# Optimization experiments

Measured on AMD Instinct MI355X. Metric: run time of the kernel, lower is better.

## Reference

```python
import jax, jax.numpy as jnp
import numpy as np

D = 6
EPS = 1e-5


def layer_norm(x, w, b):
    m = jnp.mean(x, axis=-1, keepdims=True)
    v = jnp.mean(jnp.square(x - m), axis=-1, keepdims=True)
    return (x - m) * jax.lax.rsqrt(v + EPS) * w + b


def setup_inputs() -> dict:
    key = jax.random.key(0)
    ks = jax.random.split(key, 8)
    B, S = 8192, 128
    scale = 0.2
    return {
        "x": jax.random.normal(ks[0], (B, S, D), jnp.float32),
        "ln1_w": jnp.ones((D,), jnp.float32),
        "ln1_b": jnp.zeros((D,), jnp.float32),
        "wqkv": jax.random.normal(ks[1], (D, 3 * D), jnp.float32) * scale,
        "bqkv": jnp.zeros((3 * D,), jnp.float32),
        "wo": jax.random.normal(ks[2], (D, D), jnp.float32) * scale,
        "bo": jnp.zeros((D,), jnp.float32),
        "ln2_w": jnp.ones((D,), jnp.float32),
        "ln2_b": jnp.zeros((D,), jnp.float32),
        "w1": jax.random.normal(ks[3], (D, D), jnp.float32) * scale,
        "b1": jnp.zeros((D,), jnp.float32),
        "w2": jax.random.normal(ks[4], (D, D), jnp.float32) * scale,
        "b2": jnp.zeros((D,), jnp.float32),
    }


def reference(x, ln1_w, ln1_b, wqkv, bqkv, wo, bo, ln2_w, ln2_b, w1, b1, w2, b2):
    B, S, _ = x.shape
    # --- attention sub-block: x = x + attn(ln1(x)) ---
    h = layer_norm(x, ln1_w, ln1_b)                      # [B,S,D]
    qkv = h @ wqkv + bqkv                                # [B,S,3D]
    q, k, v = jnp.split(qkv, 3, axis=-1)
    scores = jnp.einsum('bqd,bkd->bqk', q, k) / jnp.sqrt(jnp.asarray(D, x.dtype))
    causal = jnp.tril(jnp.ones((S, S), bool))            # [S,S]
    scores = jnp.where(causal, scores, jnp.asarray(-1e9, x.dtype))
    attn = jax.nn.softmax(scores, axis=-1)               # [B,S,S]
    o = jnp.einsum('bqk,bkd->bqd', attn, v) @ wo + bo
    x = x + o
    # --- FFN sub-block: x = x + W2 @ gelu(W1 @ ln2(x)) ---
    h2 = layer_norm(x, ln2_w, ln2_b)
    ff = jax.nn.gelu(h2 @ w1 + b1, approximate=False) @ w2 + b2
    return x + ff
```

## Files before the change

### kernel.cpp

```cpp
#include <hip/hip_runtime.h>
#include <cmath>


typedef float    v2f  __attribute__((ext_vector_type(2)));
typedef float    f4v  __attribute__((ext_vector_type(4)));
typedef short    s4v  __attribute__((ext_vector_type(4)));
typedef uint32_t u2   __attribute__((ext_vector_type(2)));

constexpr int D = 6;
constexpr int S = 128;
#define EPS 1e-5f
#define RSQRT_D 0.4082482904638631f
#define LOG2E   1.4426950408889634f

#define EXP2F(x) __builtin_amdgcn_exp2f(x)
#define RCPF(x)  __builtin_amdgcn_rcpf(x)
#define PKFMA(a, b, c) __builtin_elementwise_fma((a), (b), (c))

union UA { uint32_t u[2]; u2 h; s4v v; };

__device__ __forceinline__ uint32_t pkbf(float hi, float lo) {
    return __builtin_amdgcn_perm(__builtin_bit_cast(uint32_t, hi),
                                 __builtin_bit_cast(uint32_t, lo),
                                 0x07060302u);
}
__device__ __forceinline__ uint16_t bf16t(float x) {
    return (uint16_t)(__builtin_bit_cast(uint32_t, x) >> 16);
}

__device__ __forceinline__ f4v mfma16(s4v a, s4v b, f4v c) {
#if __has_builtin(__builtin_amdgcn_mfma_f32_16x16x16bf16_1k)
    return __builtin_amdgcn_mfma_f32_16x16x16bf16_1k(a, b, c, 0, 0, 0);
#else
    f4v d;
    asm volatile("v_mfma_f32_16x16x16_bf16 %0, %1, %2, %3\n\t"
                 "s_nop 7\n\ts_nop 2"
                 : "=v"(d) : "v"(a), "v"(b), "v"(c));
    return d;
#endif
}

template<int QA, int QB>
__device__ __forceinline__ void attn_pair(
    const UA (&kf)[8], const UA (&vf)[8],
    const uint32_t (*qlds)[6], float (*obuf)[10],
    int l15, int lq, int aoff)
{
    UA qfA, qfB;
    qfA.h = *(const u2*)((const char*)&qlds[QA * 16 + l15][0] + aoff);
    qfB.h = *(const u2*)((const char*)&qlds[QB * 16 + l15][0] + aoff);
    const f4v z = {0.f, 0.f, 0.f, 0.f};
    f4v OA = z, OB = z;
    #pragma unroll
    for (int jt = 0; jt <= QB; ++jt) {
        f4v cB = mfma16(kf[jt].v, qfB.v, z);
        f4v cA;
        if (jt <= QA) cA = mfma16(kf[jt].v, qfA.v, z);
        float pB0 = EXP2F(cB[0]);
        float pB1 = EXP2F(cB[1]);
        float pB2 = EXP2F(cB[2]);
        float pB3 = EXP2F(cB[3]);
        if (jt == QB) {
            pB0 = (lq * 4 + 0 > l15) ? 0.f : pB0;
            pB1 = (lq * 4 + 1 > l15) ? 0.f : pB1;
            pB2 = (lq * 4 + 2 > l15) ? 0.f : pB2;
            pB3 = (lq * 4 + 3 > l15) ? 0.f : pB3;
        }
        UA paB;
        paB.u[0] = pkbf(pB1, pB0);
        paB.u[1] = pkbf(pB3, pB2);
        OB = mfma16(paB.v, vf[jt].v, OB);
        if (jt <= QA) {
            float pA0 = EXP2F(cA[0]);
            float pA1 = EXP2F(cA[1]);
            float pA2 = EXP2F(cA[2]);
            float pA3 = EXP2F(cA[3]);
            if (jt == QA) {
                pA0 = (lq * 4 + 0 > l15) ? 0.f : pA0;
                pA1 = (lq * 4 + 1 > l15) ? 0.f : pA1;
                pA2 = (lq * 4 + 2 > l15) ? 0.f : pA2;
                pA3 = (lq * 4 + 3 > l15) ? 0.f : pA3;
            }
            UA paA;
            paA.u[0] = pkbf(pA1, pA0);
            paA.u[1] = pkbf(pA3, pA2);
            OA = mfma16(paA.v, vf[jt].v, OA);
        }
    }
    if (l15 < 7) {
        #pragma unroll
        for (int r = 0; r < 4; ++r) {
            obuf[QA * 16 + lq * 4 + r][l15] = OA[r];
            obuf[QB * 16 + lq * 4 + r][l15] = OB[r];
        }
    }
}

__global__ __launch_bounds__(S, 6) void txblock_kernel(
    const float* __restrict__ x,
    const float* __restrict__ ln1_w, const float* __restrict__ ln1_b,
    const float* __restrict__ wqkv,  const float* __restrict__ bqkv,
    const float* __restrict__ wo,    const float* __restrict__ bo,
    const float* __restrict__ ln2_w, const float* __restrict__ ln2_b,
    const float* __restrict__ w1,    const float* __restrict__ b1,
    const float* __restrict__ w2,    const float* __restrict__ b2,
    float* __restrict__ out)
{
    __shared__ uint32_t qlds[S][6];
    __shared__ uint32_t klds[S][6];
    __shared__ uint16_t vt[8][S + 8];
    __shared__ float    obuf[S][10];

    const int b = blockIdx.x;
    const int s = threadIdx.x;
    const float* xrow = x + ((size_t)b * S + s) * D;
    float*      orow = out + ((size_t)b * S + s) * D;

    v2f xv01 = ((const v2f*)xrow)[0];
    v2f xv23 = ((const v2f*)xrow)[1];
    v2f xv45 = ((const v2f*)xrow)[2];
    float xv[D] = {xv01[0], xv01[1], xv23[0], xv23[1], xv45[0], xv45[1]};

    float m = 0.f;
    #pragma unroll
    for (int d = 0; d < D; ++d) m += xv[d];
    m *= (1.0f / D);
    float var = 0.f;
    #pragma unroll
    for (int d = 0; d < D; ++d) { float t = xv[d] - m; var += t * t; }
    var *= (1.0f / D);
    float rstd = rsqrtf(var + EPS);
    float h1[D];
    #pragma unroll
    for (int d = 0; d < D; ++d)
        h1[d] = (xv[d] - m) * rstd * ln1_w[d] + ln1_b[d];

    v2f aq[3], ak[3], av[3];
    #pragma unroll
    for (int jp = 0; jp < 3; ++jp) {
        aq[jp] = ((const v2f*)bqkv)[jp];
        ak[jp] = ((const v2f*)(bqkv + D))[jp];
        av[jp] = ((const v2f*)(bqkv + 2 * D))[jp];
    }
    #pragma unroll
    for (int d = 0; d < D; ++d) {
        const float* wrow = wqkv + d * 3 * D;
        v2f hd = {h1[d], h1[d]};
        #pragma unroll
        for (int jp = 0; jp < 3; ++jp) {
            aq[jp] = PKFMA(hd, ((const v2f*)wrow)[jp], aq[jp]);
            ak[jp] = PKFMA(hd, ((const v2f*)(wrow + D))[jp], ak[jp]);
            av[jp] = PKFMA(hd, ((const v2f*)(wrow + 2 * D))[jp], av[jp]);
        }
    }
    const v2f qscale = {RSQRT_D * LOG2E, RSQRT_D * LOG2E};

    #pragma unroll
    for (int jp = 0; jp < 3; ++jp) {
        v2f qs = aq[jp] * qscale;
        qlds[s][jp] = pkbf(qs[1], qs[0]);
        klds[s][jp] = pkbf(ak[jp][1], ak[jp][0]);
    }
    qlds[s][3] = 0; qlds[s][4] = 0; qlds[s][5] = 0;
    klds[s][3] = 0; klds[s][4] = 0; klds[s][5] = 0;
    vt[0][s] = bf16t(av[0][0]);
    vt[1][s] = bf16t(av[0][1]);
    vt[2][s] = bf16t(av[1][0]);
    vt[3][s] = bf16t(av[1][1]);
    vt[4][s] = bf16t(av[2][0]);
    vt[5][s] = bf16t(av[2][1]);
    vt[6][s] = 0x3F80;
    vt[7][s] = 0;
    __syncthreads();

    const int wv  = s >> 6;
    const int l15 = s & 15;
    const int lq  = (s >> 4) & 3;
    const int aoff = (lq < 2) ? lq * 8 : 16;
    const int vne  = (l15 < 7) ? l15 : 7;

    UA kf[8], vf[8];
    #pragma unroll
    for (int jt = 0; jt < 8; ++jt) {
        kf[jt].h = *(const u2*)((const char*)&klds[jt * 16 + l15][0] + aoff);
        vf[jt].h = *(const u2*)&vt[vne][jt * 16 + lq * 4];
    }

    if (wv == 0) {
        attn_pair<0, 7>(kf, vf, qlds, obuf, l15, lq, aoff);
        attn_pair<3, 4>(kf, vf, qlds, obuf, l15, lq, aoff);
    } else {
        attn_pair<1, 6>(kf, vf, qlds, obuf, l15, lq, aoff);
        attn_pair<2, 5>(kf, vf, qlds, obuf, l15, lq, aoff);
    }
    __syncthreads();

    v2f rx01 = ((const v2f*)xrow)[0];
    v2f rx23 = ((const v2f*)xrow)[1];
    v2f rx45 = ((const v2f*)xrow)[2];

    v2f o01 = *(const v2f*)&obuf[s][0];
    v2f o23 = *(const v2f*)&obuf[s][2];
    v2f o45 = *(const v2f*)&obuf[s][4];
    float invl = RCPF(obuf[s][6]);
    v2f il = {invl, invl};
    o01 *= il; o23 *= il; o45 *= il;
    float av6[D] = {o01[0], o01[1], o23[0], o23[1], o45[0], o45[1]};

    v2f xvp[3] = {rx01, rx23, rx45};
    v2f x2p[3];
    #pragma unroll
    for (int dp = 0; dp < 3; ++dp) {
        v2f o = ((const v2f*)bo)[dp];
        #pragma unroll
        for (int e = 0; e < D; ++e) {
            v2f we = ((const v2f*)(wo + e * D))[dp];
            v2f ae = {av6[e], av6[e]};
            o = PKFMA(ae, we, o);
        }
        x2p[dp] = o + xvp[dp];
    }
    float x2[D] = {x2p[0][0], x2p[0][1], x2p[1][0], x2p[1][1], x2p[2][0], x2p[2][1]};

    float m2 = 0.f;
    #pragma unroll
    for (int d = 0; d < D; ++d) m2 += x2[d];
    m2 *= (1.0f / D);
    float var2 = 0.f;
    #pragma unroll
    for (int d = 0; d < D; ++d) { float t = x2[d] - m2; var2 += t * t; }
    var2 *= (1.0f / D);
    float rstd2 = rsqrtf(var2 + EPS);
    float h2[D];
    #pragma unroll
    for (int d = 0; d < D; ++d)
        h2[d] = (x2[d] - m2) * rstd2 * ln2_w[d] + ln2_b[d];

    v2f ap[3];
    #pragma unroll
    for (int jp = 0; jp < 3; ++jp) {
        v2f a = ((const v2f*)b1)[jp];
        #pragma unroll
        for (int d = 0; d < D; ++d) {
            v2f wd = ((const v2f*)(w1 + d * D))[jp];
            v2f hd = {h2[d], h2[d]};
            a = PKFMA(hd, wd, a);
        }
        ap[jp] = a;
    }
    float g[D];
    #pragma unroll
    for (int j = 0; j < D; ++j) {
        float a = ap[j >> 1][j & 1];
        float t  = a * a;
        float in = fmaf(0.044715f * t, a, a);
        float e  = EXP2F(in * -2.3022229f);
        float r  = RCPF(1.0f + e);
        g[j] = a * r;
    }
    #pragma unroll
    for (int dp = 0; dp < 3; ++dp) {
        v2f a = ((const v2f*)b2)[dp];
        #pragma unroll
        for (int e = 0; e < D; ++e) {
            v2f we = ((const v2f*)(w2 + e * D))[dp];
            v2f ge = {g[e], g[e]};
            a = PKFMA(ge, we, a);
        }
        ((v2f*)orow)[dp] = x2p[dp] + a;
    }
}

extern "C" void kernel_launch(void* const* d_in, const int* in_sizes, int n_in,
                              void* d_out, int out_size, void* d_ws, size_t ws_size,
                              hipStream_t stream) {
    const float* x     = (const float*)d_in[0];
    const float* ln1_w = (const float*)d_in[1];
    const float* ln1_b = (const float*)d_in[2];
    const float* wqkv  = (const float*)d_in[3];
    const float* bqkv  = (const float*)d_in[4];
    const float* wo    = (const float*)d_in[5];
    const float* bo    = (const float*)d_in[6];
    const float* ln2_w = (const float*)d_in[7];
    const float* ln2_b = (const float*)d_in[8];
    const float* w1    = (const float*)d_in[9];
    const float* b1    = (const float*)d_in[10];
    const float* w2    = (const float*)d_in[11];
    const float* b2    = (const float*)d_in[12];
    float* out = (float*)d_out;

    const int B = in_sizes[0] / (S * D);
    txblock_kernel<<<B, S, 0, stream>>>(x, ln1_w, ln1_b, wqkv, bqkv, wo, bo,
                                        ln2_w, ln2_b, w1, b1, w2, b2, out);
}
```

Baseline: 115.4 us.

## Alias output buffer onto Q/K shared memory and raise occupancy target

The obuf shared array now reuses the Q/K LDS storage, with an extra barrier once Q and K fragments are in registers, so each block uses less LDS. V fragments are loaded from LDS inside the attention loop rather than held in registers, cutting register pressure. The launch-bounds minimum is raised from 6 to 8 blocks per CU. The goal is higher occupancy, at the cost of one more __syncthreads and repeated LDS reads of V.

```diff
diff --git a/kernel.cpp b/kernel.cpp
--- a/kernel.cpp
+++ b/kernel.cpp
@@ -42,17 +42,14 @@
 
 template<int QA, int QB>
 __device__ __forceinline__ void attn_pair(
-    const UA (&kf)[8], const UA (&vf)[8],
-    const uint32_t (*qlds)[6], float (*obuf)[10],
-    int l15, int lq, int aoff)
+    const UA (&kf)[8], const uint16_t (*vt)[S + 8], int vne,
+    UA qfA, UA qfB, float (*obuf)[10], int l15, int lq)
 {
-    UA qfA, qfB;
-    qfA.h = *(const u2*)((const char*)&qlds[QA * 16 + l15][0] + aoff);
-    qfB.h = *(const u2*)((const char*)&qlds[QB * 16 + l15][0] + aoff);
     const f4v z = {0.f, 0.f, 0.f, 0.f};
     f4v OA = z, OB = z;
     #pragma unroll
     for (int jt = 0; jt <= QB; ++jt) {
+        UA vf; vf.h = *(const u2*)&vt[vne][jt * 16 + lq * 4];
         f4v cB = mfma16(kf[jt].v, qfB.v, z);
         f4v cA;
         if (jt <= QA) cA = mfma16(kf[jt].v, qfA.v, z);
@@ -69,7 +66,7 @@
         UA paB;
         paB.u[0] = pkbf(pB1, pB0);
         paB.u[1] = pkbf(pB3, pB2);
-        OB = mfma16(paB.v, vf[jt].v, OB);
+        OB = mfma16(paB.v, vf.v, OB);
         if (jt <= QA) {
             float pA0 = EXP2F(cA[0]);
             float pA1 = EXP2F(cA[1]);
@@ -84,7 +81,7 @@
             UA paA;
             paA.u[0] = pkbf(pA1, pA0);
             paA.u[1] = pkbf(pA3, pA2);
-            OA = mfma16(paA.v, vf[jt].v, OA);
+            OA = mfma16(paA.v, vf.v, OA);
         }
     }
     if (l15 < 7) {
@@ -96,7 +93,7 @@
     }
 }
 
-__global__ __launch_bounds__(S, 6) void txblock_kernel(
+__global__ __launch_bounds__(S, 8) void txblock_kernel(
     const float* __restrict__ x,
     const float* __restrict__ ln1_w, const float* __restrict__ ln1_b,
     const float* __restrict__ wqkv,  const float* __restrict__ bqkv,
@@ -106,10 +103,9 @@
     const float* __restrict__ w2,    const float* __restrict__ b2,
     float* __restrict__ out)
 {
-    __shared__ uint32_t qlds[S][6];
-    __shared__ uint32_t klds[S][6];
+    __shared__ uint32_t qk[2][S][6];
     __shared__ uint16_t vt[8][S + 8];
-    __shared__ float    obuf[S][10];
+    float (*obuf)[10] = reinterpret_cast<float(*)[10]>(&qk[0][0][0]);
 
     const int b = blockIdx.x;
     const int s = threadIdx.x;
@@ -158,11 +154,11 @@
     #pragma unroll
     for (int jp = 0; jp < 3; ++jp) {
         v2f qs = aq[jp] * qscale;
-        qlds[s][jp] = pkbf(qs[1], qs[0]);
-        klds[s][jp] = pkbf(ak[jp][1], ak[jp][0]);
-    }
-    qlds[s][3] = 0; qlds[s][4] = 0; qlds[s][5] = 0;
-    klds[s][3] = 0; klds[s][4] = 0; klds[s][5] = 0;
+        qk[0][s][jp] = pkbf(qs[1], qs[0]);
+        qk[1][s][jp] = pkbf(ak[jp][1], ak[jp][0]);
+    }
+    qk[0][s][3] = 0; qk[0][s][4] = 0; qk[0][s][5] = 0;
+    qk[1][s][3] = 0; qk[1][s][4] = 0; qk[1][s][5] = 0;
     vt[0][s] = bf16t(av[0][0]);
     vt[1][s] = bf16t(av[0][1]);
     vt[2][s] = bf16t(av[1][0]);
@@ -179,19 +175,26 @@
     const int aoff = (lq < 2) ? lq * 8 : 16;
     const int vne  = (l15 < 7) ? l15 : 7;
 
-    UA kf[8], vf[8];
-    #pragma unroll
-    for (int jt = 0; jt < 8; ++jt) {
-        kf[jt].h = *(const u2*)((const char*)&klds[jt * 16 + l15][0] + aoff);
-        vf[jt].h = *(const u2*)&vt[vne][jt * 16 + lq * 4];
-    }
+    UA kf[8];
+    #pragma unroll
+    for (int jt = 0; jt < 8; ++jt)
+        kf[jt].h = *(const u2*)((const char*)&qk[1][jt * 16 + l15][0] + aoff);
+
+    const int qt0 = wv ? 1 : 0, qt1 = wv ? 6 : 7;
+    const int qt2 = wv ? 2 : 3, qt3 = wv ? 5 : 4;
+    UA qA1, qB1, qA2, qB2;
+    qA1.h = *(const u2*)((const char*)&qk[0][qt0 * 16 + l15][0] + aoff);
+    qB1.h = *(const u2*)((const char*)&qk[0][qt1 * 16 + l15][0] + aoff);
+    qA2.h = *(const u2*)((const char*)&qk[0][qt2 * 16 + l15][0] + aoff);
+    qB2.h = *(const u2*)((const char*)&qk[0][qt3 * 16 + l15][0] + aoff);
+    __syncthreads();
 
     if (wv == 0) {
-        attn_pair<0, 7>(kf, vf, qlds, obuf, l15, lq, aoff);
-        attn_pair<3, 4>(kf, vf, qlds, obuf, l15, lq, aoff);
+        attn_pair<0, 7>(kf, vt, vne, qA1, qB1, obuf, l15, lq);
+        attn_pair<3, 4>(kf, vt, vne, qA2, qB2, obuf, l15, lq);
     } else {
-        attn_pair<1, 6>(kf, vf, qlds, obuf, l15, lq, aoff);
-        attn_pair<2, 5>(kf, vf, qlds, obuf, l15, lq, aoff);
+        attn_pair<1, 6>(kf, vt, vne, qA1, qB1, obuf, l15, lq);
+        attn_pair<2, 5>(kf, vt, vne, qA2, qB2, obuf, l15, lq);
     }
     __syncthreads();
 
```

Result: faster. 112.7 us, median of 2 (-2.3%).
